# Optimization experiments

Measured on AMD Instinct MI355X. Metric: run time of the kernel, lower is better.

## Reference

```python
import jax, jax.numpy as jnp
import numpy as np

B, N, M = 256, 50, 100
FSD, FVD, LDIM, BBD, INTER, K = 300, 2048, 2048, 128, 512, 8


def _linear(x, W, b):
    return x @ W + b


def bb_process(bb, W, b):
    # bb: [..., 4] = (x1, y1, x2, y2)
    size = bb[..., 2:] - bb[..., :2]
    centre = bb[..., :2] + 0.5 * size
    area = size[..., 0:1] * size[..., 1:2]
    shp = size[..., 0:1] / (size[..., 1:2] + 1e-14)
    feats = jnp.concatenate([bb, size, centre, area, shp], axis=-1)  # [..., 10]
    return _linear(feats, W, b)


def setup_inputs() -> dict:
    key = jax.random.key(0)
    ks = jax.random.split(key, 20)
    def nrm(k, shape, s=0.02):
        return jax.random.normal(k, shape, jnp.float32) * s
    # valid boxes: x2>x1, y2>y1
    xy_s = jax.random.uniform(ks[0], (B, N, 2)); wh_s = jax.random.uniform(ks[1], (B, N, 2))
    ps = jnp.concatenate([xy_s, xy_s + wh_s], -1)
    xy_v = jax.random.uniform(ks[2], (B, M, 2)); wh_v = jax.random.uniform(ks[3], (B, M, 2))
    pv = jnp.concatenate([xy_v, xy_v + wh_v], -1)
    return {
        "l": jax.random.normal(ks[4], (B, LDIM), jnp.float32),
        "s": jax.random.normal(ks[5], (B, N, FSD), jnp.float32),
        "ps": ps,
        "mask_s": jax.random.randint(ks[6], (B,), 1, N + 1),
        "v_ori": jax.random.normal(ks[7], (B, M, FVD), jnp.float32),
        "pv": pv,
        "mask_v": jnp.full((B,), M, dtype=jnp.int32),
        "W_bb": nrm(ks[8], (10, BBD)), "b_bb": jnp.zeros((BBD,), jnp.float32),
        "W1": nrm(ks[9], (K, BBD, INTER), 0.05),
        "W2": nrm(ks[10], (K, BBD, INTER), 0.05),
        "W_fs": nrm(ks[11], (FSD + BBD, FVD + BBD)), "b_fs": jnp.zeros((FVD + BBD,), jnp.float32),
        "W_l2": nrm(ks[12], (LDIM, FVD + BBD)), "b_l2": jnp.zeros((FVD + BBD,), jnp.float32),
        "W_l3": nrm(ks[13], (LDIM, FVD + BBD)), "b_l3": jnp.zeros((FVD + BBD,), jnp.float32),
        "W_fv": nrm(ks[14], (FVD + BBD, FVD + BBD)), "b_fv": jnp.zeros((FVD + BBD,), jnp.float32),
        "W_o1": nrm(ks[15], (BBD + FVD, FSD)), "b_o1": jnp.zeros((FSD,), jnp.float32),
        "W_o2": nrm(ks[16], (BBD + FVD, FVD)), "b_o2": jnp.zeros((FVD,), jnp.float32),
        "epsilon": jax.random.normal(ks[17], (), jnp.float32),
    }


def reference(l, s, ps, mask_s, v_ori, pv, mask_v,
              W_bb, b_bb, W1, W2, W_fs, b_fs, W_l2, b_l2, W_l3, b_l3,
              W_fv, b_fv, W_o1, b_o1, W_o2, b_o2, epsilon):
    # eval mode: no dropout, no cooling noise. it=1 (only valid setting), penalty_ratio=10.
    s_bb = bb_process(ps, W_bb, b_bb)            # [B,N,BBD]
    v_bb = bb_process(pv, W_bb, b_bb)            # [B,M,BBD]
    v = jnp.concatenate([v_ori, v_bb], -1)       # [B,M,FVD+BBD]
    lq = l[:, None, :]                           # [B,1,LDIM]
    token_mask = jnp.arange(N)[None, :] < mask_s[:, None]   # [B,N] bool
    out_mask = token_mask[:, :, None].astype(s.dtype)        # [B,N,1]
    # K-head bilinear adjacency over bounding-box embeddings
    s_f = jnp.einsum('bnd,kdi->bkni', s_bb, W1)  # [B,K,N,INTER]
    v_f = jnp.einsum('bmd,kdi->bkmi', v_bb, W2)  # [B,K,M,INTER]
    adj = jnp.einsum('bkni,bkmi->bnm', s_f, v_f) / K  # mean over heads
    adj = jax.nn.softmax(adj, axis=2)
    # cooling: pow(relu(adj), 1/0.25) then renormalize
    adj = jax.nn.relu(adj) ** 4.0
    adj = adj / jnp.sum(adj, axis=-1, keepdims=True)
    adj = adj * out_mask                          # [B,N,M]
    # gated message sources
    prepared_s = jax.nn.relu(_linear(
        _linear(jnp.concatenate([s, s_bb], -1), W_fs, b_fs) * _linear(lq, W_l3, b_l3),
        W_o2, b_o2))                              # [B,N,FVD]
    prepared_v = jax.nn.relu(_linear(
        _linear(v, W_fv, b_fv) * jax.nn.softmax(_linear(lq, W_l2, b_l2), axis=-1),
        W_o1, b_o1))                              # [B,M,FSD]
    # masked matmul aggregation
    new_ele = jnp.einsum('bnm,bnd->bmd', adj, prepared_s)   # [B,M,FVD]
    v_out = epsilon * new_ele + v_ori
    s_out = jnp.concatenate([s, jnp.einsum('bnm,bmd->bnd', adj, prepared_v)], -1)  # [B,N,2*FSD]
    adj_inf = jnp.where(token_mask[:, :, None], adj, -jnp.inf)  # adj + inf_tmp
    fro = jnp.sum(jnp.linalg.norm(adj, axis=-1), axis=-1) / mask_s.astype(jnp.float32)
    loss = -jnp.sum(fro) / 10.0                   # att_loss / penalty_ratio
    return (s_out * out_mask, v_out, adj_inf, loss)
```

## Files before the change

### kernel.cpp

```cpp
#include <hip/hip_runtime.h>
#include <math.h>

#define B_ 256
#define N_ 50
#define M_ 100
#define FSD_ 300
#define FVD_ 2048
#define LDIM_ 2048
#define BBD_ 128
#define INTER_ 512
#define K_ 8
#define DFS_ 428
#define DV_ 2176
#define NEGBIG_ (-3.0e38f)

typedef __attribute__((ext_vector_type(8))) short bf16x8_t;
typedef __attribute__((ext_vector_type(4))) float f32x4_t;

__device__ __forceinline__ unsigned short f2bf(float x) {
  union { float f; unsigned int u; } c; c.f = x;
  unsigned int r = c.u + 0x7FFFu + ((c.u >> 16) & 1u);
  return (unsigned short)(r >> 16);
}

__device__ __forceinline__ void gload16(const void* g, void* l) {
  __builtin_amdgcn_global_load_lds(
      (const __attribute__((address_space(1))) void*)g,
      (__attribute__((address_space(3))) void*)l, 16, 0, 0);
}

__global__ __launch_bounds__(128) void bb_kernel(const float* __restrict__ pbox,
                                                 const float* __restrict__ W_bb,
                                                 const float* __restrict__ b_bb,
                                                 float* __restrict__ outbb) {
  int row = blockIdx.x;
  int o = threadIdx.x;
  const float* p = pbox + (size_t)row * 4;
  float x0 = p[0], y0 = p[1], x1 = p[2], y1 = p[3];
  float sx = x1 - x0, sy = y1 - y0;
  float f[10] = {x0, y0, x1, y1, sx, sy, x0 + 0.5f * sx, y0 + 0.5f * sy,
                 sx * sy, sx / (sy + 1e-14f)};
  float acc = b_bb[o];
#pragma unroll
  for (int i = 0; i < 10; i++) acc += f[i] * W_bb[i * BBD_ + o];
  outbb[(size_t)row * BBD_ + o] = acc;
}

__global__ __launch_bounds__(128) void wq_kernel(const float* __restrict__ W1,
                                                 const float* __restrict__ W2,
                                                 float* __restrict__ Wq) {
  int d = blockIdx.x, e = threadIdx.x;
  __shared__ float w1row[INTER_];
  float acc = 0.f;
  for (int k = 0; k < K_; k++) {
    __syncthreads();
    for (int i = e; i < INTER_; i += 128) w1row[i] = W1[((size_t)k * BBD_ + d) * INTER_ + i];
    __syncthreads();
    const float* w2 = W2 + ((size_t)k * BBD_ + e) * INTER_;
#pragma unroll 8
    for (int i = 0; i < INTER_; i++) acc += w1row[i] * w2[i];
  }
  Wq[d * BBD_ + e] = acc * (1.0f / K_);
}

__global__ __launch_bounds__(128) void t_kernel(const float* __restrict__ s_bb,
                                                const float* __restrict__ Wq,
                                                float* __restrict__ t) {
  int row = blockIdx.x, e = threadIdx.x;
  __shared__ float srow[BBD_];
  srow[e] = s_bb[(size_t)row * BBD_ + e];
  __syncthreads();
  float acc = 0;
#pragma unroll 8
  for (int d = 0; d < BBD_; d++) acc += srow[d] * Wq[d * BBD_ + e];
  t[(size_t)row * BBD_ + e] = acc;
}

__global__ __launch_bounds__(128) void adjdot_kernel(const float* __restrict__ t,
                                                     const float* __restrict__ v_bb,
                                                     float* __restrict__ adjw) {
  int row = blockIdx.x;
  int b = row / N_;
  int tid = threadIdx.x;
  __shared__ float tS[BBD_];
  tS[tid] = t[(size_t)row * BBD_ + tid];
  __syncthreads();
  if (tid < M_) {
    const float4* vr = (const float4*)(v_bb + ((size_t)b * M_ + tid) * BBD_);
    const float4* tr = (const float4*)tS;
    float acc = 0.f;
#pragma unroll 8
    for (int d4 = 0; d4 < BBD_ / 4; d4++) {
      float4 vv = vr[d4];
      float4 tt = tr[d4];
      acc += tt.x * vv.x + tt.y * vv.y + tt.z * vv.z + tt.w * vv.w;
    }
    adjw[(size_t)row * M_ + tid] = acc * 4.0f;
  }
}

__global__ __launch_bounds__(64) void adjsm_kernel(float* __restrict__ adjw,
                                                   const int* __restrict__ mask_s,
                                                   float* __restrict__ adj_inf,
                                                   float* __restrict__ lossbuf) {
  int row = blockIdx.x;
  int b = row / N_, n = row % N_;
  int tid = threadIdx.x;
  float* xr = adjw + (size_t)row * M_;
  int i1 = tid + 64;
  float v0 = xr[tid];
  float v1 = (i1 < M_) ? xr[i1] : -INFINITY;
  float mx = fmaxf(v0, v1);
#pragma unroll
  for (int off = 32; off > 0; off >>= 1) mx = fmaxf(mx, __shfl_xor(mx, off));
  float e0 = __expf(v0 - mx);
  float e1 = (i1 < M_) ? __expf(v1 - mx) : 0.f;
  float sm = e0 + e1;
#pragma unroll
  for (int off = 32; off > 0; off >>= 1) sm += __shfl_xor(sm, off);
  float inv = 1.0f / sm;
  int msk = mask_s[b];
  bool live = n < msk;
  float a0 = live ? e0 * inv : 0.f;
  float a1 = live ? e1 * inv : 0.f;
  xr[tid] = a0;
  adj_inf[(size_t)row * M_ + tid] = live ? a0 : NEGBIG_;
  if (i1 < M_) {
    xr[i1] = a1;
    adj_inf[(size_t)row * M_ + i1] = live ? a1 : NEGBIG_;
  }
  float n2 = a0 * a0 + a1 * a1;
#pragma unroll
  for (int off = 32; off > 0; off >>= 1) n2 += __shfl_xor(n2, off);
  if (tid == 0) lossbuf[row] = sqrtf(n2) / (float)msk;
}

__global__ __launch_bounds__(256) void lossred_kernel(const float* __restrict__ lossbuf,
                                                      float* __restrict__ loss) {
  int tid = threadIdx.x;
  float s = 0;
  for (int i = tid; i < B_ * N_; i += 256) s += lossbuf[i];
  __shared__ float red[4];
#pragma unroll
  for (int off = 32; off > 0; off >>= 1) s += __shfl_xor(s, off);
  if ((tid & 63) == 0) red[tid >> 6] = s;
  __syncthreads();
  if (tid == 0) loss[0] = -(red[0] + red[1] + red[2] + red[3]) / 10.0f;
}

__global__ __launch_bounds__(256) void softmax_kernel(float* __restrict__ g) {
  __shared__ float buf[DV_];
  __shared__ float red[4];
  __shared__ float bc;
  int b = blockIdx.x, tid = threadIdx.x;
  float* row = g + (size_t)b * DV_;
  float mx = -INFINITY;
  for (int i = tid; i < DV_; i += 256) {
    float v = row[i];
    buf[i] = v;
    mx = fmaxf(mx, v);
  }
#pragma unroll
  for (int off = 32; off > 0; off >>= 1) mx = fmaxf(mx, __shfl_xor(mx, off));
  if ((tid & 63) == 0) red[tid >> 6] = mx;
  __syncthreads();
  if (tid == 0) bc = fmaxf(fmaxf(red[0], red[1]), fmaxf(red[2], red[3]));
  __syncthreads();
  mx = bc;
  float sm = 0;
  for (int i = tid; i < DV_; i += 256) {
    float e = __expf(buf[i] - mx);
    buf[i] = e;
    sm += e;
  }
#pragma unroll
  for (int off = 32; off > 0; off >>= 1) sm += __shfl_xor(sm, off);
  if ((tid & 63) == 0) red[tid >> 6] = sm;
  __syncthreads();
  if (tid == 0) bc = red[0] + red[1] + red[2] + red[3];
  __syncthreads();
  float inv = 1.0f / bc;
  for (int i = tid; i < DV_; i += 256) row[i] = buf[i] * inv;
}

__global__ __launch_bounds__(256) void wtrans_kernel(const float* __restrict__ W,
                                                     unsigned short* __restrict__ Wt,
                                                     int K, int N, int Kpad) {
  __shared__ float tile[32][33];
  int n0 = blockIdx.x * 32, k0 = blockIdx.y * 32;
  int tj = threadIdx.x & 31, ti0 = threadIdx.x >> 5;
#pragma unroll
  for (int s = 0; s < 4; ++s) {
    int ki = k0 + ti0 + s * 8;
    int nj = n0 + tj;
    tile[ti0 + s * 8][tj] = (ki < K && nj < N) ? W[(size_t)ki * N + nj] : 0.f;
  }
  __syncthreads();
#pragma unroll
  for (int s = 0; s < 4; ++s) {
    int nloc = ti0 + s * 8;
    Wt[(size_t)(n0 + nloc) * Kpad + k0 + tj] = f2bf(tile[tj][nloc]);
  }
}

__global__ __launch_bounds__(256) void cat2bf_kernel(const float* __restrict__ A0, int ca,
                                                     const float* __restrict__ A1, int cb,
                                                     unsigned short* __restrict__ dst,
                                                     int cpad) {
  int row = blockIdx.y;
  int c4 = (blockIdx.x * 256 + threadIdx.x) * 4;
  if (c4 >= cpad) return;
  float4 v = make_float4(0.f, 0.f, 0.f, 0.f);
  if (c4 < ca)
    v = *(const float4*)(A0 + (size_t)row * ca + c4);
  else if (c4 < ca + cb)
    v = *(const float4*)(A1 + (size_t)row * cb + (c4 - ca));
  unsigned long long p = (unsigned long long)f2bf(v.x) |
                         ((unsigned long long)f2bf(v.y) << 16) |
                         ((unsigned long long)f2bf(v.z) << 32) |
                         ((unsigned long long)f2bf(v.w) << 48);
  *(unsigned long long*)(dst + (size_t)row * cpad + c4) = p;
}

template <int EPI, bool OBF>
__global__ __launch_bounds__(256) void mfma_gemm(
    const unsigned short* __restrict__ A, const unsigned short* __restrict__ Bt,
    const float* __restrict__ bias, const float* __restrict__ gate,
    void* __restrict__ Cout, int Kpad, int Ncols, int NStore, int ldc, int rows_per_b) {
  __shared__ unsigned short As[128 * 64];
  __shared__ unsigned short Bs[128 * 64];
  int tid = threadIdx.x;
  int wid = tid >> 6, lane = tid & 63;
  int wm = wid >> 1, wn = wid & 1;
  int lr = lane & 15, lh = lane >> 4;
  int row0 = blockIdx.y * 128, col0 = blockIdx.x * 128;

  f32x4_t acc[4][4];
#pragma unroll
  for (int m = 0; m < 4; ++m)
#pragma unroll
    for (int n = 0; n < 4; ++n) acc[m][n] = (f32x4_t){0.f, 0.f, 0.f, 0.f};

  int sr[4], sj[4];
#pragma unroll
  for (int c = 0; c < 4; ++c) {
    int b = ((c * 4 + wid) << 10) + lane * 16;
    sr[c] = b >> 7;
    sj[c] = ((b & 127) ^ ((sr[c] & 7) << 4)) >> 1;
  }

  int nK = Kpad >> 6;
  for (int kt = 0; kt < nK; ++kt) {
    int k0 = kt << 6;
#pragma unroll
    for (int c = 0; c < 4; ++c) {
      gload16(A + (size_t)(row0 + sr[c]) * Kpad + k0 + sj[c], &As[(c * 4 + wid) << 9]);
      gload16(Bt + (size_t)(col0 + sr[c]) * Kpad + k0 + sj[c], &Bs[(c * 4 + wid) << 9]);
    }
    __syncthreads();
    bf16x8_t af[4][2], bf[4][2];
#pragma unroll
    for (int m = 0; m < 4; ++m) {
      int rl = wm * 64 + m * 16 + lr;
      int sw = (rl & 7) << 4;
#pragma unroll
      for (int kk = 0; kk < 2; ++kk) {
        int inner = ((kk * 64 + lh * 16) ^ sw) >> 1;
        af[m][kk] = *(const bf16x8_t*)&As[rl * 64 + inner];
      }
    }
#pragma unroll
    for (int n = 0; n < 4; ++n) {
      int nl = wn * 64 + n * 16 + lr;
      int sw = (nl & 7) << 4;
#pragma unroll
      for (int kk = 0; kk < 2; ++kk) {
        int inner = ((kk * 64 + lh * 16) ^ sw) >> 1;
        bf[n][kk] = *(const bf16x8_t*)&Bs[nl * 64 + inner];
      }
    }
#pragma unroll
    for (int m = 0; m < 4; ++m)
#pragma unroll
      for (int n = 0; n < 4; ++n) {
        acc[m][n] = __builtin_amdgcn_mfma_f32_16x16x32_bf16(af[m][0], bf[n][0], acc[m][n], 0, 0, 0);
        acc[m][n] = __builtin_amdgcn_mfma_f32_16x16x32_bf16(af[m][1], bf[n][1], acc[m][n], 0, 0, 0);
      }
    __syncthreads();
  }

#pragma unroll
  for (int m = 0; m < 4; ++m) {
    int gr0 = row0 + wm * 64 + m * 16 + lh * 4;
#pragma unroll
    for (int n = 0; n < 4; ++n) {
      int gc = col0 + wn * 64 + n * 16 + lr;
      if (gc >= NStore) continue;
      float bv = bias[gc];
      f32x4_t v = acc[m][n];
#pragma unroll
      for (int i = 0; i < 4; ++i) {
        int gr = gr0 + i;
        float x = v[i] + bv;
        if constexpr (EPI == 1) x *= gate[(size_t)(gr / rows_per_b) * Ncols + gc];
        if constexpr (EPI == 2) x = fmaxf(x, 0.f);
        if constexpr (OBF)
          ((unsigned short*)Cout)[(size_t)gr * ldc + gc] = f2bf(x);
        else
          ((float*)Cout)[(size_t)gr * ldc + gc] = x;
      }
    }
  }
}

__global__ __launch_bounds__(128) void outv_kernel(const float* __restrict__ adjw,
                                                   const float* __restrict__ ps_prep,
                                                   const float* __restrict__ v_ori,
                                                   const float* __restrict__ eps_p,
                                                   float* __restrict__ v_out) {
  int b = blockIdx.x;
  int ch = blockIdx.y;
  int tid = threadIdx.x;
  __shared__ float psc[N_][128];
  float eps = eps_p[0];
  for (int n = 0; n < N_; n++)
    psc[n][tid] = ps_prep[((size_t)b * N_ + n) * FVD_ + ch * 128 + tid];
  __syncthreads();
  const float* ab = adjw + (size_t)b * N_ * M_;
  for (int m0 = 0; m0 < M_; m0 += 4) {
    float a0 = 0, a1 = 0, a2 = 0, a3 = 0;
    for (int n = 0; n < N_; n++) {
      float p = psc[n][tid];
      a0 += ab[n * M_ + m0] * p;
      a1 += ab[n * M_ + m0 + 1] * p;
      a2 += ab[n * M_ + m0 + 2] * p;
      a3 += ab[n * M_ + m0 + 3] * p;
    }
    size_t base = ((size_t)b * M_ + m0) * FVD_ + (size_t)ch * 128 + tid;
    v_out[base] = eps * a0 + v_ori[base];
    v_out[base + FVD_] = eps * a1 + v_ori[base + FVD_];
    v_out[base + 2 * FVD_] = eps * a2 + v_ori[base + 2 * FVD_];
    v_out[base + 3 * FVD_] = eps * a3 + v_ori[base + 3 * FVD_];
  }
}

__global__ __launch_bounds__(256) void outs_kernel(const float* __restrict__ s,
                                                   const float* __restrict__ adjw,
                                                   const float* __restrict__ pv_prep,
                                                   const int* __restrict__ mask_s,
                                                   float* __restrict__ s_out) {
  int row = blockIdx.x;
  int b = row / N_, n = row % N_;
  int tid = threadIdx.x;
  __shared__ float arow[M_];
  bool live = n < mask_s[b];
  if (!live) {
    for (int d = tid; d < 2 * FSD_; d += 256) s_out[(size_t)row * 2 * FSD_ + d] = 0.f;
    return;
  }
  if (tid < M_) arow[tid] = adjw[(size_t)row * M_ + tid];
  __syncthreads();
  for (int d = tid; d < FSD_; d += 256)
    s_out[(size_t)row * 2 * FSD_ + d] = s[(size_t)row * FSD_ + d];
  for (int d = tid; d < FSD_; d += 256) {
    float acc = 0.f;
#pragma unroll 4
    for (int m = 0; m < M_; m++) acc += arow[m] * pv_prep[((size_t)b * M_ + m) * FSD_ + d];
    s_out[(size_t)row * 2 * FSD_ + FSD_ + d] = acc;
  }
}

extern "C" void kernel_launch(void* const* d_in, const int* in_sizes, int n_in,
                              void* d_out, int out_size, void* d_ws, size_t ws_size,
                              hipStream_t stream) {
  (void)in_sizes; (void)n_in; (void)out_size; (void)ws_size;
  const float* l = (const float*)d_in[0];
  const float* s = (const float*)d_in[1];
  const float* ps_box = (const float*)d_in[2];
  const int* mask_s = (const int*)d_in[3];
  const float* v_ori = (const float*)d_in[4];
  const float* pv_box = (const float*)d_in[5];
  const float* W_bb = (const float*)d_in[7];
  const float* b_bb = (const float*)d_in[8];
  const float* W1 = (const float*)d_in[9];
  const float* W2 = (const float*)d_in[10];
  const float* W_fs = (const float*)d_in[11];
  const float* b_fs = (const float*)d_in[12];
  const float* W_l2 = (const float*)d_in[13];
  const float* b_l2 = (const float*)d_in[14];
  const float* W_l3 = (const float*)d_in[15];
  const float* b_l3 = (const float*)d_in[16];
  const float* W_fv = (const float*)d_in[17];
  const float* b_fv = (const float*)d_in[18];
  const float* W_o1 = (const float*)d_in[19];
  const float* b_o1 = (const float*)d_in[20];
  const float* W_o2 = (const float*)d_in[21];
  const float* b_o2 = (const float*)d_in[22];
  const float* eps = (const float*)d_in[23];

  float* ws = (float*)d_ws;
  float* s_bb = ws;
  float* v_bb = s_bb + 1638400;
  float* Wq = v_bb + 3276800;
  float* t = Wq + 16384;
  float* adjw = t + 1638400;
  float* lossbuf = adjw + 1280000;
  float* g3 = lossbuf + 12800;
  float* g2 = g3 + 557056;
  float* ps_prep = g2 + 557056;
  float* pv_prep = ps_prep + 26214400;
  unsigned short* bfb = (unsigned short*)(pv_prep + 7680000);
  unsigned short* R1 = bfb;
  unsigned short* R2 = R1 + 55705600;
  unsigned short* Wt_fs = R2 + 55705600;
  unsigned short* Wt_o2 = Wt_fs + 974848;
  unsigned short* Wt_fv = Wt_o2 + 4456448;
  unsigned short* Wt_o1 = Wt_fv + 4734976;
  unsigned short* Wt_l2 = Wt_o1 + 835584;
  unsigned short* Wt_l3 = Wt_l2 + 4456448;
  unsigned short* A_l = Wt_l3 + 4456448;
  unsigned short* A_fv = R1;
  unsigned short* A_fs = R1;
  unsigned short* h_bf = R1 + 8000000;
  unsigned short* y_bf = R2;

  float* out = (float*)d_out;
  float* o_sout = out;
  float* o_vout = out + 7680000;
  float* o_adjinf = out + 60108800;
  float* o_loss = out + 61388800;

  bb_kernel<<<B_ * N_, 128, 0, stream>>>(ps_box, W_bb, b_bb, s_bb);
  bb_kernel<<<B_ * M_, 128, 0, stream>>>(pv_box, W_bb, b_bb, v_bb);
  wq_kernel<<<BBD_, 128, 0, stream>>>(W1, W2, Wq);
  t_kernel<<<B_ * N_, 128, 0, stream>>>(s_bb, Wq, t);
  adjdot_kernel<<<B_ * N_, 128, 0, stream>>>(t, v_bb, adjw);
  adjsm_kernel<<<B_ * N_, 64, 0, stream>>>(adjw, mask_s, o_adjinf, lossbuf);
  lossred_kernel<<<1, 256, 0, stream>>>(lossbuf, o_loss);

  wtrans_kernel<<<dim3(68, 64), 256, 0, stream>>>(W_l3, Wt_l3, LDIM_, DV_, 2048);
  wtrans_kernel<<<dim3(68, 64), 256, 0, stream>>>(W_l2, Wt_l2, LDIM_, DV_, 2048);
  wtrans_kernel<<<dim3(68, 68), 256, 0, stream>>>(W_fv, Wt_fv, DV_, DV_, 2176);
  wtrans_kernel<<<dim3(12, 68), 256, 0, stream>>>(W_o1, Wt_o1, DV_, FSD_, 2176);
  wtrans_kernel<<<dim3(68, 14), 256, 0, stream>>>(W_fs, Wt_fs, DFS_, DV_, 448);
  wtrans_kernel<<<dim3(64, 68), 256, 0, stream>>>(W_o2, Wt_o2, DV_, FVD_, 2176);
  cat2bf_kernel<<<dim3(2, B_), 256, 0, stream>>>(l, LDIM_, nullptr, 0, A_l, 2048);

  mfma_gemm<0, false><<<dim3(17, 2), 256, 0, stream>>>(A_l, Wt_l3, b_l3, nullptr, g3,
                                                       2048, DV_, DV_, DV_, 1);
  mfma_gemm<0, false><<<dim3(17, 2), 256, 0, stream>>>(A_l, Wt_l2, b_l2, nullptr, g2,
                                                       2048, DV_, DV_, DV_, 1);
  softmax_kernel<<<B_, 256, 0, stream>>>(g2);

  cat2bf_kernel<<<dim3(3, B_ * M_), 256, 0, stream>>>(v_ori, FVD_, v_bb, BBD_, A_fv, 2176);
  mfma_gemm<1, true><<<dim3(17, 200), 256, 0, stream>>>(A_fv, Wt_fv, b_fv, g2, y_bf,
                                                        2176, DV_, DV_, DV_, M_);
  mfma_gemm<2, false><<<dim3(3, 200), 256, 0, stream>>>(y_bf, Wt_o1, b_o1, nullptr, pv_prep,
                                                        2176, DV_, FSD_, FSD_, 1);

  cat2bf_kernel<<<dim3(1, B_ * N_), 256, 0, stream>>>(s, FSD_, s_bb, BBD_, A_fs, 448);
  mfma_gemm<1, true><<<dim3(17, 100), 256, 0, stream>>>(A_fs, Wt_fs, b_fs, g3, h_bf,
                                                        448, DV_, DV_, DV_, N_);
  mfma_gemm<2, false><<<dim3(16, 100), 256, 0, stream>>>(h_bf, Wt_o2, b_o2, nullptr, ps_prep,
                                                         2176, FVD_, FVD_, FVD_, 1);

  outv_kernel<<<dim3(B_, 16), 128, 0, stream>>>(adjw, ps_prep, v_ori, eps, o_vout);
  outs_kernel<<<B_ * N_, 256, 0, stream>>>(s, adjw, pv_prep, mask_s, o_sout);
}
```

Before: 2.171 ms.

## Register-tile outv and outs aggregation kernels with shared-memory adjacency reuse

```diff
diff --git a/kernel.cpp b/kernel.cpp
--- a/kernel.cpp
+++ b/kernel.cpp
@@ -258,7 +258,7 @@
       gload16(Bt + (size_t)(col0 + sr[c]) * Kpad + k0 + sj[c], &Bs[(c * 4 + wid) << 9]);
     }
     __syncthreads();
-    bf16x8_t af[4][2], bf[4][2];
+    bf16x8_t af[4][2], bfr[4][2];
 #pragma unroll
     for (int m = 0; m < 4; ++m) {
       int rl = wm * 64 + m * 16 + lr;
@@ -276,15 +276,15 @@
 #pragma unroll
       for (int kk = 0; kk < 2; ++kk) {
         int inner = ((kk * 64 + lh * 16) ^ sw) >> 1;
-        bf[n][kk] = *(const bf16x8_t*)&Bs[nl * 64 + inner];
+        bfr[n][kk] = *(const bf16x8_t*)&Bs[nl * 64 + inner];
       }
     }
 #pragma unroll
     for (int m = 0; m < 4; ++m)
 #pragma unroll
       for (int n = 0; n < 4; ++n) {
-        acc[m][n] = __builtin_amdgcn_mfma_f32_16x16x32_bf16(af[m][0], bf[n][0], acc[m][n], 0, 0, 0);
-        acc[m][n] = __builtin_amdgcn_mfma_f32_16x16x32_bf16(af[m][1], bf[n][1], acc[m][n], 0, 0, 0);
+        acc[m][n] = __builtin_amdgcn_mfma_f32_16x16x32_bf16(af[m][0], bfr[n][0], acc[m][n], 0, 0, 0);
+        acc[m][n] = __builtin_amdgcn_mfma_f32_16x16x32_bf16(af[m][1], bfr[n][1], acc[m][n], 0, 0, 0);
       }
     __syncthreads();
   }
@@ -322,25 +322,34 @@
   int ch = blockIdx.y;
   int tid = threadIdx.x;
   __shared__ float psc[N_][128];
+  __shared__ float adjs[N_ * M_];
+  for (int i = tid; i < N_ * 128; i += 128) {
+    int n = i >> 7, c = i & 127;
+    psc[n][c] = ps_prep[((size_t)b * N_ + n) * FVD_ + ch * 128 + c];
+  }
+  for (int i = tid; i < N_ * M_; i += 128) adjs[i] = adjw[(size_t)b * N_ * M_ + i];
+  __syncthreads();
   float eps = eps_p[0];
-  for (int n = 0; n < N_; n++)
-    psc[n][tid] = ps_prep[((size_t)b * N_ + n) * FVD_ + ch * 128 + tid];
-  __syncthreads();
-  const float* ab = adjw + (size_t)b * N_ * M_;
-  for (int m0 = 0; m0 < M_; m0 += 4) {
-    float a0 = 0, a1 = 0, a2 = 0, a3 = 0;
-    for (int n = 0; n < N_; n++) {
-      float p = psc[n][tid];
-      a0 += ab[n * M_ + m0] * p;
-      a1 += ab[n * M_ + m0 + 1] * p;
-      a2 += ab[n * M_ + m0 + 2] * p;
-      a3 += ab[n * M_ + m0 + 3] * p;
-    }
-    size_t base = ((size_t)b * M_ + m0) * FVD_ + (size_t)ch * 128 + tid;
-    v_out[base] = eps * a0 + v_ori[base];
-    v_out[base + FVD_] = eps * a1 + v_ori[base + FVD_];
-    v_out[base + 2 * FVD_] = eps * a2 + v_ori[base + 2 * FVD_];
-    v_out[base + 3 * FVD_] = eps * a3 + v_ori[base + 3 * FVD_];
+  int col4 = (tid & 31) * 4;
+  int mbase = (tid >> 5) * 25;
+  for (int mb = 0; mb < 25; mb += 5) {
+    f32x4_t acc[5];
+#pragma unroll
+    for (int q = 0; q < 5; ++q) acc[q] = (f32x4_t){0.f, 0.f, 0.f, 0.f};
+    const float* arow = adjs + mbase + mb;
+#pragma unroll 2
+    for (int n = 0; n < N_; ++n) {
+      f32x4_t p = *(const f32x4_t*)&psc[n][col4];
+#pragma unroll
+      for (int q = 0; q < 5; ++q) acc[q] += arow[n * M_ + q] * p;
+    }
+#pragma unroll
+    for (int q = 0; q < 5; ++q) {
+      int m = mbase + mb + q;
+      size_t base = ((size_t)b * M_ + m) * FVD_ + ch * 128 + col4;
+      f32x4_t vo = *(const f32x4_t*)&v_ori[base];
+      *(f32x4_t*)&v_out[base] = eps * acc[q] + vo;
+    }
   }
 }
 
@@ -349,24 +358,39 @@
                                                    const float* __restrict__ pv_prep,
                                                    const int* __restrict__ mask_s,
                                                    float* __restrict__ s_out) {
-  int row = blockIdx.x;
-  int b = row / N_, n = row % N_;
-  int tid = threadIdx.x;
-  __shared__ float arow[M_];
-  bool live = n < mask_s[b];
-  if (!live) {
-    for (int d = tid; d < 2 * FSD_; d += 256) s_out[(size_t)row * 2 * FSD_ + d] = 0.f;
-    return;
-  }
-  if (tid < M_) arow[tid] = adjw[(size_t)row * M_ + tid];
-  __syncthreads();
-  for (int d = tid; d < FSD_; d += 256)
-    s_out[(size_t)row * 2 * FSD_ + d] = s[(size_t)row * FSD_ + d];
-  for (int d = tid; d < FSD_; d += 256) {
-    float acc = 0.f;
-#pragma unroll 4
-    for (int m = 0; m < M_; m++) acc += arow[m] * pv_prep[((size_t)b * M_ + m) * FSD_ + d];
-    s_out[(size_t)row * 2 * FSD_ + FSD_ + d] = acc;
+  int b = blockIdx.x;
+  int c0 = blockIdx.y * 64;
+  int tid = threadIdx.x;
+  __shared__ float pvc[M_ * 64];
+  __shared__ float adjs[52 * M_];
+  for (int i = tid; i < M_ * 64; i += 256) {
+    int m = i >> 6, c = c0 + (i & 63);
+    pvc[i] = (c < FSD_) ? pv_prep[((size_t)b * M_ + m) * FSD_ + c] : 0.f;
+  }
+  for (int i = tid; i < 52 * M_; i += 256)
+    adjs[i] = (i < N_ * M_) ? adjw[(size_t)b * N_ * M_ + i] : 0.f;
+  __syncthreads();
+  int col = tid & 63, ngrp = tid >> 6;
+  int msk = mask_s[b];
+  float acc[13];
+#pragma unroll
+  for (int i = 0; i < 13; ++i) acc[i] = 0.f;
+  for (int m = 0; m < M_; ++m) {
+    float pv = pvc[m * 64 + col];
+#pragma unroll
+    for (int i = 0; i < 13; ++i) acc[i] += adjs[(ngrp * 13 + i) * M_ + m] * pv;
+  }
+  int gc = c0 + col;
+  if (gc < FSD_) {
+#pragma unroll
+    for (int i = 0; i < 13; ++i) {
+      int n = ngrp * 13 + i;
+      if (n >= N_) break;
+      size_t row = (size_t)b * N_ + n;
+      bool live = n < msk;
+      s_out[row * (2 * FSD_) + gc] = live ? s[row * FSD_ + gc] : 0.f;
+      s_out[row * (2 * FSD_) + FSD_ + gc] = acc[i];
+    }
   }
 }
 
@@ -465,5 +489,5 @@
                                                          2176, FVD_, FVD_, FVD_, 1);
 
   outv_kernel<<<dim3(B_, 16), 128, 0, stream>>>(adjw, ps_prep, v_ori, eps, o_vout);
-  outs_kernel<<<B_ * N_, 256, 0, stream>>>(s, adjw, pv_prep, mask_s, o_sout);
-}
+  outs_kernel<<<dim3(B_, 5), 256, 0, stream>>>(s, adjw, pv_prep, mask_s, o_sout);
+}
```

After: 1.792 ms. -17.4%, faster.
